# Optimization experiments

Hardware: AMD Instinct MI355X
Metric: run time of the kernel (lower is better)

The kernel has to match this reference:

```python
import jax, jax.numpy as jnp
import numpy as np

NUM_HEADS = 8
NUM_LEVELS = 4
NUM_POINTS = 4


def setup_inputs() -> dict:
    key = jax.random.key(0)
    kq, kp, kv, k1, k2, k3, k4 = jax.random.split(key, 7)
    B, Q, C = 4, 4096, 256
    M, L, P = NUM_HEADS, NUM_LEVELS, NUM_POINTS
    shapes_np = np.array([[128, 128], [64, 64], [32, 32], [16, 16]], dtype=np.int32)
    sizes = shapes_np[:, 0] * shapes_np[:, 1]
    N = int(sizes.sum())  # 21760
    level_index = jnp.asarray(np.concatenate([[0], np.cumsum(sizes)[:-1]]).astype(np.int32))
    q = jax.random.normal(kq, (B, Q, C), jnp.float32)
    p = jax.random.uniform(kp, (B, Q, L, 2), jnp.float32)  # normalized ref points
    v = jax.random.normal(kv, (B, N, C), jnp.float32)
    # proj_offset bias: radial grid init from reset_parameters()
    t = np.arange(M, dtype=np.float32) * (2.0 * np.pi / M)
    grid = np.stack([np.cos(t), np.sin(t)], -1)
    grid = grid / np.abs(grid).max(-1, keepdims=True)
    grid = np.tile(grid[:, None, None, :], (1, L, P, 1)) * np.arange(1, P + 1, dtype=np.float32)[None, None, :, None]
    b_off = jnp.asarray(grid.reshape(-1))
    s = 1.0 / np.sqrt(C).astype(np.float32)
    W_off = jax.random.normal(k1, (C, M * L * P * 2), jnp.float32) * 0.01
    W_attn = jax.random.normal(k2, (C, M * L * P), jnp.float32) * s
    b_attn = jnp.zeros((M * L * P,), jnp.float32)
    W_val = jax.random.normal(k3, (C, C), jnp.float32) * s
    b_val = jnp.zeros((C,), jnp.float32)
    W_out = jax.random.normal(k4, (C, C), jnp.float32) * s
    b_out = jnp.zeros((C,), jnp.float32)
    return {"q": q, "p": p, "v": v, "shapes": jnp.asarray(shapes_np), "level_index": level_index,
            "W_off": W_off, "b_off": b_off, "W_attn": W_attn, "b_attn": b_attn,
            "W_val": W_val, "b_val": b_val, "W_out": W_out, "b_out": b_out}


def _ms_deform_attn(q, p, v, shapes, level_index, W_off, b_off, W_attn, b_attn, W_val, b_val, W_out, b_out):
    B, Q, C = q.shape
    M, L, P = NUM_HEADS, NUM_LEVELS, NUM_POINTS
    D = C // M
    N = v.shape[1]
    # value projection -> [B, M, N, D] (head-major for gather)
    v_p = (v @ W_val + b_val).reshape(B, N, M, D).transpose(0, 2, 1, 3)
    # attention weights, softmax over L*P (classic MSDeformAttn kernel contract)
    attn = jax.nn.softmax((q @ W_attn + b_attn).reshape(B, Q, M, L * P), axis=-1)
    attn = attn.reshape(B, Q, M, L, P)
    # sampling locations (P==2 reference-point branch)
    off = (q @ W_off + b_off).reshape(B, Q, M, L, P, 2)
    norm = jnp.stack([shapes[:, 1], shapes[:, 0]], -1).astype(jnp.float32)  # (W, H) per level
    loc = p[:, :, None, :, None, :] + off / norm[None, None, None, :, None, :]  # [B,Q,M,L,P,2]

    out = jnp.zeros((B, M, Q, D), jnp.float32)
    for l in range(L):
        Hf = shapes[l, 0].astype(jnp.float32)
        Wf = shapes[l, 1].astype(jnp.float32)
        Hi = shapes[l, 0]
        Wi = shapes[l, 1]
        base = level_index[l]
        # grid_sample(align_corners=False) convention: pixel = loc*size - 0.5
        x = loc[:, :, :, l, :, 0] * Wf - 0.5  # [B,Q,M,P]
        y = loc[:, :, :, l, :, 1] * Hf - 0.5
        x0 = jnp.floor(x)
        y0 = jnp.floor(y)
        lx, ly = x - x0, y - y0
        x0i = x0.astype(jnp.int32)
        y0i = y0.astype(jnp.int32)

        def corner(xi, yi, w):
            valid = (xi >= 0) & (xi < Wi) & (yi >= 0) & (yi < Hi)
            idx = base + jnp.clip(yi, 0, Hi - 1) * Wi + jnp.clip(xi, 0, Wi - 1)  # [B,Q,M,P]
            idx = idx.transpose(0, 2, 1, 3).reshape(B, M, Q * P)
            g = jnp.take_along_axis(v_p, idx[..., None], axis=2).reshape(B, M, Q, P, D)
            wv = (w * valid.astype(w.dtype)).transpose(0, 2, 1, 3)[..., None]  # [B,M,Q,P,1]
            return g * wv

        samp = (corner(x0i, y0i, (1 - lx) * (1 - ly))
                + corner(x0i + 1, y0i, lx * (1 - ly))
                + corner(x0i, y0i + 1, (1 - lx) * ly)
                + corner(x0i + 1, y0i + 1, lx * ly))  # [B,M,Q,P,D]
        a_l = attn[:, :, :, l, :].transpose(0, 2, 1, 3)  # [B,M,Q,P]
        out = out + jnp.einsum('bmqpd,bmqp->bmqd', samp, a_l)

    out = out.transpose(0, 2, 1, 3).reshape(B, Q, M * D)
    return out @ W_out + b_out


def reference(q, p, v, shapes, level_index, W_off, b_off, W_attn, b_attn, W_val, b_val, W_out, b_out):
    return _ms_deform_attn(q, p, v, shapes, level_index, W_off, b_off, W_attn, b_attn, W_val, b_val, W_out, b_out)
```

## Files before the change

kernel.cpp:

```cpp
#include <hip/hip_runtime.h>
#include <cstddef>

#define BB 4
#define QQ 4096
#define MM 8
#define NN 21760

typedef __bf16 bf16_8 __attribute__((ext_vector_type(8)));
typedef __bf16 bf16_4 __attribute__((ext_vector_type(4)));
typedef float  floatx4 __attribute__((ext_vector_type(4)));

__global__ __launch_bounds__(256) void prep_weights(
    const float* __restrict__ Wv, const float* __restrict__ Wa,
    const float* __restrict__ Wo, const float* __restrict__ Wu,
    const float* __restrict__ ba, const float* __restrict__ bo,
    __bf16* __restrict__ Wt, float* __restrict__ biasq)
{
    const int gid = blockIdx.x * 256 + threadIdx.x;
    if (gid < 65536) {
        const int n = gid >> 8, k = gid & 255;
        Wt[gid] = (__bf16)Wv[k * 256 + n];
    } else if (gid < 163840) {
        const int o = gid - 65536;
        const int n = o >> 8, k = o & 255;
        Wt[gid] = (__bf16)(n < 128 ? Wa[k * 128 + n] : Wo[k * 256 + (n - 128)]);
    } else if (gid < 229376) {
        const int o = gid - 163840;
        const int n = o >> 8, k = o & 255;
        Wt[gid] = (__bf16)Wu[k * 256 + n];
    } else if (gid < 229760) {
        const int j = gid - 229376;
        biasq[j] = (j < 128) ? ba[j] : bo[j - 128];
    }
}

__global__ __launch_bounds__(512, 4) void gemm_vq4(
    const float* __restrict__ v,
    const float* __restrict__ q,
    const __bf16* __restrict__ Wt,
    const float* __restrict__ b_val,
    const float* __restrict__ biasq,
    __bf16* __restrict__ vpb,
    float* __restrict__ gqp)
{
    __shared__ __bf16 As[2][64][128];

    const int tid  = threadIdx.x;
    const int lane = tid & 63;
    const int wave = tid >> 6;
    const int quad = lane >> 4;
    const int l16  = lane & 15;
    const int flat = blockIdx.x;

    const bool is_vp = (flat >= 384);
    int z = 0, tb, colep;
    const float* Arow;
    const __bf16* Wpan;
    if (is_vp) {
        const int bi = flat - 384;
        z  = bi / 170;
        tb = (bi - z * 170) * 128;
        Arow  = v + (size_t)z * NN * 256;
        Wpan  = Wt;
        colep = wave * 32;
    } else {
        const int g0 = flat * 2;
        const int slice = g0 >> 8;
        tb = (g0 & 255) * 64;
        Arow  = q;
        Wpan  = Wt + 65536 + (size_t)(slice * 128) * 256;
        colep = slice * 128 + wave * 16;
    }

    float4 a4[4];
    auto issue = [&](int ph) {
        const int tile = ph >> 1, h = ph & 1;
        #pragma unroll
        for (int c = 0; c < 4; ++c) {
            const int cid = c * 512 + tid;
            const int rr  = cid >> 5;
            const int kc  = (cid & 31) * 4;
            a4[c] = *(const float4*)(Arow + (size_t)(tb + tile * 64 + rr) * 256
                                      + h * 128 + kc);
        }
    };
    auto wr = [&](int ph) {
        const int buf = ph & 1;
        #pragma unroll
        for (int c = 0; c < 4; ++c) {
            const int cid = c * 512 + tid;
            const int rr  = cid >> 5;
            const int kc  = (cid & 31) * 4;
            bf16_4 w;
            w[0] = (__bf16)a4[c].x; w[1] = (__bf16)a4[c].y;
            w[2] = (__bf16)a4[c].z; w[3] = (__bf16)a4[c].w;
            const int col = ((((kc >> 3) ^ (rr & 7)) << 3) | (kc & 7));
            *(bf16_4*)&As[buf][rr][col] = w;
        }
    };

    issue(0);

    bf16_8 wf0[8], wf1[8];
    #pragma unroll
    for (int kk = 0; kk < 8; ++kk) {
        wf0[kk] = *(const bf16_8*)(Wpan + (size_t)(colep % 384 - (is_vp ? 0 : (colep - wave * 16 - (colep >= 128 ? (colep >= 256 ? 256 : 128) : 0))) * 0 + 0) * 0
                                    + 0);
    }
    {
        const int wrow0 = is_vp ? (wave * 32) : (wave * 16);
        #pragma unroll
        for (int kk = 0; kk < 8; ++kk) {
            wf0[kk] = *(const bf16_8*)(Wpan + (size_t)(wrow0 + l16) * 256 + kk * 32 + quad * 8);
            if (is_vp)
                wf1[kk] = *(const bf16_8*)(Wpan + (size_t)(wrow0 + 16 + l16) * 256 + kk * 32 + quad * 8);
        }
    }

    wr(0);
    issue(1);
    asm volatile("s_waitcnt lgkmcnt(0)" ::: "memory");
    __builtin_amdgcn_s_barrier();

    floatx4 acc0[4], acc1[4];
    #pragma unroll
    for (int p = 0; p < 4; ++p) {
        if ((p & 1) == 0) {
            #pragma unroll
            for (int it = 0; it < 4; ++it) { acc0[it] = (floatx4){0,0,0,0}; acc1[it] = (floatx4){0,0,0,0}; }
        }
        {
            const int buf = p & 1, h = p & 1;
            #pragma unroll
            for (int k2 = 0; k2 < 4; ++k2) {
                const int kk = h * 4 + k2;
                bf16_8 af[4];
                #pragma unroll
                for (int it = 0; it < 4; ++it)
                    af[it] = *(const bf16_8*)&As[buf][it * 16 + l16]
                                               [(((k2 * 4 + quad) ^ (l16 & 7)) << 3)];
                #pragma unroll
                for (int it = 0; it < 4; ++it) {
                    acc0[it] = __builtin_amdgcn_mfma_f32_16x16x32_bf16(wf0[kk], af[it], acc0[it], 0, 0, 0);
                    if (is_vp)
                        acc1[it] = __builtin_amdgcn_mfma_f32_16x16x32_bf16(wf1[kk], af[it], acc1[it], 0, 0, 0);
                }
            }
        }
        if (p & 1) {
            const int tile = p >> 1;
            const int tok0 = tb + tile * 64;
            if (is_vp) {
                #pragma unroll
                for (int j = 0; j < 2; ++j) {
                    const int n0 = colep + j * 16 + quad * 4;
                    const float4 b4 = *(const float4*)(b_val + n0);
                    const int mh = n0 >> 5, dd = n0 & 31;
                    #pragma unroll
                    for (int it = 0; it < 4; ++it) {
                        const int token = tok0 + it * 16 + l16;
                        const floatx4 av = j ? acc1[it] : acc0[it];
                        bf16_4 ob;
                        ob[0] = (__bf16)(av[0] + b4.x);
                        ob[1] = (__bf16)(av[1] + b4.y);
                        ob[2] = (__bf16)(av[2] + b4.z);
                        ob[3] = (__bf16)(av[3] + b4.w);
                        *(bf16_4*)(vpb + (((size_t)z * 8 + mh) * NN + token) * 32 + dd) = ob;
                    }
                }
            } else {
                const int n0 = colep + quad * 4;
                const float4 b4 = *(const float4*)(biasq + n0);
                #pragma unroll
                for (int it = 0; it < 4; ++it) {
                    const int token = tok0 + it * 16 + l16;
                    float4 ot;
                    ot.x = acc0[it][0] + b4.x;
                    ot.y = acc0[it][1] + b4.y;
                    ot.z = acc0[it][2] + b4.z;
                    ot.w = acc0[it][3] + b4.w;
                    *(float4*)(gqp + (size_t)token * 384 + n0) = ot;
                }
            }
        }
        if (p < 3) {
            wr(p + 1);
            if (p < 2) issue(p + 2);
            asm volatile("s_waitcnt lgkmcnt(0)" ::: "memory");
            __builtin_amdgcn_s_barrier();
        }
    }
}

template<typename AT, int NCB, int MODE>
__global__ __launch_bounds__(512, 4) void gemm_ws(
    const AT* __restrict__ A,
    const __bf16* __restrict__ Wn,
    const float* __restrict__ bias,
    void* __restrict__ Cout,
    int tokens, int ldc)
{
    constexpr int F  = NCB / 8;
    constexpr int NJ = F / 16;

    const int z    = blockIdx.z;
    const int col0 = blockIdx.x * NCB;
    const AT* Ab   = A + (size_t)z * tokens * 256;
    const __bf16* Wb = Wn + (size_t)col0 * 256;

    __shared__ __bf16 As[64][256];

    const int tid  = threadIdx.x;
    const int lane = tid & 63;
    const int wave = tid >> 6;
    const int quad = lane >> 4;
    const int l16  = lane & 15;
    const int wave_f = wave * F;

    const int token0 = blockIdx.y * 64;
    if (sizeof(AT) == 4) {
        const float* Af = (const float*)Ab;
        #pragma unroll
        for (int c = 0; c < 8; ++c) {
            const int cid = c * 512 + tid;
            const int r   = cid >> 6;
            const int kc  = (cid & 63) * 4;
            const float4 av = *(const float4*)(Af + (size_t)(token0 + r) * 256 + kc);
            bf16_4 w;
            w[0] = (__bf16)av.x; w[1] = (__bf16)av.y;
            w[2] = (__bf16)av.z; w[3] = (__bf16)av.w;
            const int col = ((((kc >> 3) ^ (r & 7)) << 3) | (kc & 7));
            *(bf16_4*)&As[r][col] = w;
        }
    } else {
        const __bf16* Ah = (const __bf16*)Ab;
        #pragma unroll
        for (int c = 0; c < 4; ++c) {
            const int cid = c * 512 + tid;
            const int r   = cid >> 5;
            const int kc  = (cid & 31) * 8;
            const bf16_8 av = *(const bf16_8*)(Ah + (size_t)(token0 + r) * 256 + kc);
            const int col = (((kc >> 3) ^ (r & 7)) << 3);
            *(bf16_8*)&As[r][col] = av;
        }
    }

    bf16_8 wf[8][NJ];
    #pragma unroll
    for (int kk = 0; kk < 8; ++kk)
        #pragma unroll
        for (int j = 0; j < NJ; ++j)
            wf[kk][j] = *(const bf16_8*)(Wb + (size_t)(wave_f + j * 16 + l16) * 256
                                          + kk * 32 + quad * 8);
    __syncthreads();

    floatx4 acc[NJ][4] = {};
    #pragma unroll
    for (int kk = 0; kk < 8; ++kk) {
        bf16_8 af[4];
        #pragma unroll
        for (int it = 0; it < 4; ++it)
            af[it] = *(const bf16_8*)&As[it * 16 + l16]
                                       [(((kk * 4 + quad) ^ (l16 & 7)) << 3)];
        #pragma unroll
        for (int j = 0; j < NJ; ++j)
            #pragma unroll
            for (int it = 0; it < 4; ++it)
                acc[j][it] = __builtin_amdgcn_mfma_f32_16x16x32_bf16(wf[kk][j], af[it], acc[j][it], 0, 0, 0);
    }

    #pragma unroll
    for (int j = 0; j < NJ; ++j) {
        const int n0 = col0 + wave_f + j * 16 + quad * 4;
        const float4 b4 = *(const float4*)(bias + n0);
        #pragma unroll
        for (int it = 0; it < 4; ++it) {
            const int token = token0 + it * 16 + l16;
            const float v0 = acc[j][it][0] + b4.x;
            const float v1 = acc[j][it][1] + b4.y;
            const float v2 = acc[j][it][2] + b4.z;
            const float v3 = acc[j][it][3] + b4.w;
            if (MODE == 0) {
                float4 o; o.x = v0; o.y = v1; o.z = v2; o.w = v3;
                *(float4*)((float*)Cout + ((size_t)z * tokens + token) * ldc + n0) = o;
            } else {
                const int mh = n0 >> 5, dd = n0 & 31;
                bf16_4 ob;
                ob[0] = (__bf16)v0; ob[1] = (__bf16)v1; ob[2] = (__bf16)v2; ob[3] = (__bf16)v3;
                *(bf16_4*)((__bf16*)Cout + (((size_t)z * 8 + mh) * NN + token) * 32 + dd) = ob;
            }
        }
    }
}

__device__ __forceinline__ float bflo(unsigned u) { return __uint_as_float(u << 16); }
__device__ __forceinline__ float bfhi(unsigned u) { return __uint_as_float(u & 0xffff0000u); }

__global__ __launch_bounds__(512) void sampler(
    const __bf16* __restrict__ vp,
    const float* __restrict__ gqp,
    const float* __restrict__ pref,
    __bf16* __restrict__ mid)
{
    const int t    = threadIdx.x;
    const int m    = t >> 6;
    const int lane = t & 63;
    const int s    = lane >> 2;
    const int c    = lane & 3;
    const int l    = s >> 2;
    const int bq   = blockIdx.x;
    const int b    = bq >> 12;

    const int   Hi = 128 >> l;
    const float Hf = (float)Hi;
    const int   base = (l == 0) ? 0 : (l == 1) ? 16384 : (l == 2) ? 20480 : 21504;

    const float logit = gqp[(size_t)bq * 384 + m * 16 + s];
    const float e = __expf(logit);
    float sum = e;
    #pragma unroll
    for (int k = 4; k < 64; k <<= 1) sum += __shfl_xor(sum, k, 64);
    const float a = e * __builtin_amdgcn_rcpf(sum);

    const float2 off = *(const float2*)(gqp + (size_t)bq * 384 + 128 + (m * 16 + s) * 2);
    const float2 pr  = *(const float2*)(pref + (size_t)bq * 8 + l * 2);

    const float x = fmaf(pr.x, Hf, off.x - 0.5f);
    const float y = fmaf(pr.y, Hf, off.y - 0.5f);
    const float x0f = floorf(x), y0f = floorf(y);
    const float lx = x - x0f, ly = y - y0f;
    const int x0 = (int)x0f, y0 = (int)y0f;
    const int cx0 = min(max(x0, 0), Hi - 1), cx1 = min(max(x0 + 1, 0), Hi - 1);
    const int cy0 = min(max(y0, 0), Hi - 1), cy1 = min(max(y0 + 1, 0), Hi - 1);
    const bool vx0 = (x0 >= 0) && (x0 < Hi), vx1 = (x0 + 1 >= 0) && (x0 + 1 < Hi);
    const bool vy0 = (y0 >= 0) && (y0 < Hi), vy1 = (y0 + 1 >= 0) && (y0 + 1 < Hi);
    const float w00 = a * (1.f - lx) * (1.f - ly) * ((vx0 && vy0) ? 1.f : 0.f);
    const float w10 = a * lx * (1.f - ly) * ((vx1 && vy0) ? 1.f : 0.f);
    const float w01 = a * (1.f - lx) * ly * ((vx0 && vy1) ? 1.f : 0.f);
    const float w11 = a * lx * ly * ((vx1 && vy1) ? 1.f : 0.f);

    const __bf16* vbase = vp + ((size_t)b * 8 + m) * NN * 32;
    const uint4 u00 = *((const uint4*)(vbase + (size_t)(base + cy0 * Hi + cx0) * 32) + c);
    const uint4 u10 = *((const uint4*)(vbase + (size_t)(base + cy0 * Hi + cx1) * 32) + c);
    const uint4 u01 = *((const uint4*)(vbase + (size_t)(base + cy1 * Hi + cx0) * 32) + c);
    const uint4 u11 = *((const uint4*)(vbase + (size_t)(base + cy1 * Hi + cx1) * 32) + c);

    float f[8];
    f[0] = w00*bflo(u00.x) + w10*bflo(u10.x) + w01*bflo(u01.x) + w11*bflo(u11.x);
    f[1] = w00*bfhi(u00.x) + w10*bfhi(u10.x) + w01*bfhi(u01.x) + w11*bfhi(u11.x);
    f[2] = w00*bflo(u00.y) + w10*bflo(u10.y) + w01*bflo(u01.y) + w11*bflo(u11.y);
    f[3] = w00*bfhi(u00.y) + w10*bfhi(u10.y) + w01*bfhi(u01.y) + w11*bfhi(u11.y);
    f[4] = w00*bflo(u00.z) + w10*bflo(u10.z) + w01*bflo(u01.z) + w11*bflo(u11.z);
    f[5] = w00*bfhi(u00.z) + w10*bfhi(u10.z) + w01*bfhi(u01.z) + w11*bfhi(u11.z);
    f[6] = w00*bflo(u00.w) + w10*bflo(u10.w) + w01*bflo(u01.w) + w11*bflo(u11.w);
    f[7] = w00*bfhi(u00.w) + w10*bfhi(u10.w) + w01*bfhi(u01.w) + w11*bfhi(u11.w);

    const int b2 = (lane >> 2) & 1, b3 = (lane >> 3) & 1, b4i = (lane >> 4) & 1;
    #pragma unroll
    for (int j = 0; j < 4; ++j) {
        const float sel  = b2 ? f[j] : f[j + 4];
        const float recv = __shfl_xor(sel, 4, 64);
        f[j] = (b2 ? f[j + 4] : f[j]) + recv;
    }
    #pragma unroll
    for (int j = 0; j < 2; ++j) {
        const float sel  = b3 ? f[j] : f[j + 2];
        const float recv = __shfl_xor(sel, 8, 64);
        f[j] = (b3 ? f[j + 2] : f[j]) + recv;
    }
    {
        const float sel  = b4i ? f[0] : f[1];
        const float recv = __shfl_xor(sel, 16, 64);
        f[0] = (b4i ? f[1] : f[0]) + recv;
    }
    f[0] += __shfl_xor(f[0], 32, 64);

    if (!(lane & 32)) {
        const int chan = (c << 3) | (b2 << 2) | (b3 << 1) | b4i;
        mid[(size_t)bq * 256 + m * 32 + chan] = (__bf16)f[0];
    }
}

extern "C" void kernel_launch(void* const* d_in, const int* in_sizes, int n_in,
                              void* d_out, int out_size, void* d_ws, size_t ws_size,
                              hipStream_t stream) {
    const float* q      = (const float*)d_in[0];
    const float* p      = (const float*)d_in[1];
    const float* v      = (const float*)d_in[2];
    const float* W_off  = (const float*)d_in[5];
    const float* b_off  = (const float*)d_in[6];
    const float* W_attn = (const float*)d_in[7];
    const float* b_attn = (const float*)d_in[8];
    const float* W_val  = (const float*)d_in[9];
    const float* b_val  = (const float*)d_in[10];
    const float* W_out  = (const float*)d_in[11];
    const float* b_out  = (const float*)d_in[12];
    float* out = (float*)d_out;

    float*  gqp   = (float*)d_ws;
    float*  biasq = gqp + (size_t)16384 * 384;
    __bf16* mid   = (__bf16*)(biasq + 384);
    __bf16* vpb   = mid + (size_t)16384 * 256;
    __bf16* Wt    = vpb + (size_t)BB * 8 * NN * 32;
    __bf16* Wt_out = Wt + 163840;

    prep_weights<<<898, 256, 0, stream>>>(W_val, W_attn, W_off, W_out, b_attn, b_off, Wt, biasq);

    gemm_vq4<<<1064, 512, 0, stream>>>(v, q, Wt, b_val, biasq, vpb, gqp);

    sampler<<<BB * QQ, 512, 0, stream>>>(vpb, gqp, p, mid);

    {
        dim3 grid(2, 256, 1);
        gemm_ws<__bf16, 128, 0><<<grid, 512, 0, stream>>>(mid, Wt_out, b_out, out, BB * QQ, 256);
    }
}
```

Before: 296.2 us.

## Split value-projection GEMM blocks across two column halves and stream weight fragments

After: 249.0 us. -15.9%, faster.

```diff
diff --git a/kernel.cpp b/kernel.cpp
--- a/kernel.cpp
+++ b/kernel.cpp
@@ -34,7 +34,7 @@
     }
 }
 
-__global__ __launch_bounds__(512, 4) void gemm_vq4(
+__global__ __launch_bounds__(512, 4) void gemm_vq6(
     const float* __restrict__ v,
     const float* __restrict__ q,
     const __bf16* __restrict__ Wt,
@@ -57,12 +57,14 @@
     const float* Arow;
     const __bf16* Wpan;
     if (is_vp) {
-        const int bi = flat - 384;
-        z  = bi / 170;
-        tb = (bi - z * 170) * 128;
+        const int bi   = flat - 384;
+        const int ch   = bi & 1;
+        const int rest = bi >> 1;
+        z  = rest / 170;
+        tb = (rest - z * 170) * 128;
         Arow  = v + (size_t)z * NN * 256;
-        Wpan  = Wt;
-        colep = wave * 32;
+        Wpan  = Wt + (size_t)(ch * 128) * 256;
+        colep = ch * 128 + wave * 16;
     } else {
         const int g0 = flat * 2;
         const int slice = g0 >> 8;
@@ -71,6 +73,7 @@
         Wpan  = Wt + 65536 + (size_t)(slice * 128) * 256;
         colep = slice * 128 + wave * 16;
     }
+    const int wrow = wave * 16 + l16;
 
     float4 a4[4];
     auto issue = [&](int ph) {
@@ -100,73 +103,54 @@
     };
 
     issue(0);
-
-    bf16_8 wf0[8], wf1[8];
-    #pragma unroll
-    for (int kk = 0; kk < 8; ++kk) {
-        wf0[kk] = *(const bf16_8*)(Wpan + (size_t)(colep % 384 - (is_vp ? 0 : (colep - wave * 16 - (colep >= 128 ? (colep >= 256 ? 256 : 128) : 0))) * 0 + 0) * 0
-                                    + 0);
-    }
-    {
-        const int wrow0 = is_vp ? (wave * 32) : (wave * 16);
-        #pragma unroll
-        for (int kk = 0; kk < 8; ++kk) {
-            wf0[kk] = *(const bf16_8*)(Wpan + (size_t)(wrow0 + l16) * 256 + kk * 32 + quad * 8);
-            if (is_vp)
-                wf1[kk] = *(const bf16_8*)(Wpan + (size_t)(wrow0 + 16 + l16) * 256 + kk * 32 + quad * 8);
-        }
-    }
-
     wr(0);
     issue(1);
     asm volatile("s_waitcnt lgkmcnt(0)" ::: "memory");
     __builtin_amdgcn_s_barrier();
 
-    floatx4 acc0[4], acc1[4];
+    floatx4 acc[4];
     #pragma unroll
     for (int p = 0; p < 4; ++p) {
-        if ((p & 1) == 0) {
+        const int h = p & 1;
+
+        bf16_8 wfp[4];
+        #pragma unroll
+        for (int k2 = 0; k2 < 4; ++k2)
+            wfp[k2] = *(const bf16_8*)(Wpan + (size_t)wrow * 256
+                                        + (h * 4 + k2) * 32 + quad * 8);
+
+        if (h == 0) {
             #pragma unroll
-            for (int it = 0; it < 4; ++it) { acc0[it] = (floatx4){0,0,0,0}; acc1[it] = (floatx4){0,0,0,0}; }
-        }
-        {
-            const int buf = p & 1, h = p & 1;
+            for (int it = 0; it < 4; ++it) acc[it] = (floatx4){0, 0, 0, 0};
+        }
+
+        #pragma unroll
+        for (int k2 = 0; k2 < 4; ++k2) {
+            bf16_8 af[4];
             #pragma unroll
-            for (int k2 = 0; k2 < 4; ++k2) {
-                const int kk = h * 4 + k2;
-                bf16_8 af[4];
-                #pragma unroll
-                for (int it = 0; it < 4; ++it)
-                    af[it] = *(const bf16_8*)&As[buf][it * 16 + l16]
-                                               [(((k2 * 4 + quad) ^ (l16 & 7)) << 3)];
+            for (int it = 0; it < 4; ++it)
+                af[it] = *(const bf16_8*)&As[p & 1][it * 16 + l16]
+                                           [(((k2 * 4 + quad) ^ (l16 & 7)) << 3)];
+            #pragma unroll
+            for (int it = 0; it < 4; ++it)
+                acc[it] = __builtin_amdgcn_mfma_f32_16x16x32_bf16(wfp[k2], af[it], acc[it], 0, 0, 0);
+        }
+
+        if (h) {
+            const int tok0 = tb + (p >> 1) * 64;
+            if (is_vp) {
+                const int n0 = colep + quad * 4;
+                const float4 b4 = *(const float4*)(b_val + n0);
+                const int mh = n0 >> 5, dd = n0 & 31;
                 #pragma unroll
                 for (int it = 0; it < 4; ++it) {
-                    acc0[it] = __builtin_amdgcn_mfma_f32_16x16x32_bf16(wf0[kk], af[it], acc0[it], 0, 0, 0);
-                    if (is_vp)
-                        acc1[it] = __builtin_amdgcn_mfma_f32_16x16x32_bf16(wf1[kk], af[it], acc1[it], 0, 0, 0);
-                }
-            }
-        }
-        if (p & 1) {
-            const int tile = p >> 1;
-            const int tok0 = tb + tile * 64;
-            if (is_vp) {
-                #pragma unroll
-                for (int j = 0; j < 2; ++j) {
-                    const int n0 = colep + j * 16 + quad * 4;
-                    const float4 b4 = *(const float4*)(b_val + n0);
-                    const int mh = n0 >> 5, dd = n0 & 31;
-                    #pragma unroll
-                    for (int it = 0; it < 4; ++it) {
-                        const int token = tok0 + it * 16 + l16;
-                        const floatx4 av = j ? acc1[it] : acc0[it];
-                        bf16_4 ob;
-                        ob[0] = (__bf16)(av[0] + b4.x);
-                        ob[1] = (__bf16)(av[1] + b4.y);
-                        ob[2] = (__bf16)(av[2] + b4.z);
-                        ob[3] = (__bf16)(av[3] + b4.w);
-                        *(bf16_4*)(vpb + (((size_t)z * 8 + mh) * NN + token) * 32 + dd) = ob;
-                    }
+                    const int token = tok0 + it * 16 + l16;
+                    bf16_4 ob;
+                    ob[0] = (__bf16)(acc[it][0] + b4.x);
+                    ob[1] = (__bf16)(acc[it][1] + b4.y);
+                    ob[2] = (__bf16)(acc[it][2] + b4.z);
+                    ob[3] = (__bf16)(acc[it][3] + b4.w);
+                    *(bf16_4*)(vpb + (((size_t)z * 8 + mh) * NN + token) * 32 + dd) = ob;
                 }
             } else {
                 const int n0 = colep + quad * 4;
@@ -175,14 +159,15 @@
                 for (int it = 0; it < 4; ++it) {
                     const int token = tok0 + it * 16 + l16;
                     float4 ot;
-                    ot.x = acc0[it][0] + b4.x;
-                    ot.y = acc0[it][1] + b4.y;
-                    ot.z = acc0[it][2] + b4.z;
-                    ot.w = acc0[it][3] + b4.w;
+                    ot.x = acc[it][0] + b4.x;
+                    ot.y = acc[it][1] + b4.y;
+                    ot.z = acc[it][2] + b4.z;
+                    ot.w = acc[it][3] + b4.w;
                     *(float4*)(gqp + (size_t)token * 384 + n0) = ot;
                 }
             }
         }
+
         if (p < 3) {
             wr(p + 1);
             if (p < 2) issue(p + 2);
@@ -406,7 +391,7 @@
 
     prep_weights<<<898, 256, 0, stream>>>(W_val, W_attn, W_off, W_out, b_attn, b_off, Wt, biasq);
 
-    gemm_vq4<<<1064, 512, 0, stream>>>(v, q, Wt, b_val, biasq, vpb, gqp);
+    gemm_vq6<<<1744, 512, 0, stream>>>(v, q, Wt, b_val, biasq, vpb, gqp);
 
     sampler<<<BB * QQ, 512, 0, stream>>>(vpb, gqp, p, mid);
 
```
